# Optimization experiments

Hardware: AMD Instinct MI355X
Metric: run time of the kernel (lower is better)

Reference implementation:

```python
import jax, jax.numpy as jnp
import numpy as np

N, E, D, H = 50000, 800000, 64, 4


def setup_inputs() -> dict:
    key = jax.random.key(0)
    ks = jax.random.split(key, 12)
    w = lambda k, shape: jax.random.normal(k, shape, jnp.float32) * 0.05
    return {
        "nfeats": jax.random.normal(ks[0], (N, D), jnp.float32),
        "efeats": jax.random.normal(ks[1], (E, D), jnp.float32),
        "src": jax.random.randint(ks[2], (E,), 0, N),
        "dst": jax.random.randint(ks[3], (E,), 0, N),
        "W_ni": w(ks[4], (D, H * D)),
        "W_nj": w(ks[5], (D, H * D)),
        "W_fij": w(ks[6], (D, H * D)),
        "bias_e": jnp.zeros((H * D,), jnp.float32),
        "attn": w(ks[7], (H, D)),
        "W_src": w(ks[8], (D, H * D)),
        "W_mlp_node": w(ks[9], (H * D, D)),
        "b_mlp_node": jnp.zeros((D,), jnp.float32),
        "W_mlp_edge": w(ks[10], (H * D, D)),
        "b_mlp_edge": jnp.zeros((D,), jnp.float32),
    }


def reference(nfeats, efeats, src, dst, W_ni, W_nj, W_fij, bias_e, attn,
              W_src, W_mlp_node, b_mlp_node, W_mlp_edge, b_mlp_edge):
    n, d = nfeats.shape
    h = attn.shape[0]
    # DGL EGATConv: edge logits from src node, dst node and edge features
    f_ni = (nfeats @ W_ni)[src]            # [E, H*D] gather src
    f_nj = (nfeats @ W_nj)[dst]            # [E, H*D] gather dst
    f_fij = efeats @ W_fij                 # [E, H*D]
    f_out = jax.nn.leaky_relu(f_ni + f_nj + f_fij + bias_e, 0.01)
    f_out = f_out.reshape(-1, h, d)        # [E, H, D] new edge feats
    e = jnp.einsum('ehd,hd->eh', f_out, attn)  # [E, H] attention logits
    # edge softmax over incoming edges of each dst node
    e_max = jax.ops.segment_max(e, dst, num_segments=n)
    e_exp = jnp.exp(e - e_max[dst])
    denom = jax.ops.segment_sum(e_exp, dst, num_segments=n)
    a = e_exp / denom[dst]                 # [E, H]
    # weighted message passing: scatter-sum to dst
    h_src = (nfeats @ W_src).reshape(n, h, d)[src]  # [E, H, D]
    h_out = jax.ops.segment_sum(h_src * a[:, :, None], dst, num_segments=n)  # [N, H, D]
    # EGATLayer head-mixing MLPs + ELU
    node = jax.nn.elu(h_out.reshape(n, h * d) @ W_mlp_node + b_mlp_node)
    edge = jax.nn.elu(f_out.reshape(-1, h * d) @ W_mlp_edge + b_mlp_edge)
    return node, edge
```

## Files before the change

kernel.cpp:

```cpp
#include <hip/hip_runtime.h>
#include <hip/hip_bf16.h>

#define N_NODES 50000
#define N_EDGES 800000
#define DD 64
#define HH 4
#define HD 256
#define EB 32
#define CAP 64

typedef __attribute__((ext_vector_type(8))) short bf16x8;
typedef __attribute__((ext_vector_type(4))) float f32x4;

__device__ __forceinline__ short f2bf(float x) {
  unsigned u = __builtin_bit_cast(unsigned, x);
  unsigned r = (u + 0x7fffu + ((u >> 16) & 1u)) >> 16;
  return (short)r;
}
__device__ __forceinline__ float bf2f(unsigned short u) {
  return __builtin_bit_cast(float, (unsigned)u << 16);
}

__global__ __launch_bounds__(256) void k_proj(const float* __restrict__ nfeats,
    const float* __restrict__ W_src, unsigned short* __restrict__ hsrc) {
  __shared__ __align__(16) float Wl[DD * HD];
  const float4* W4 = (const float4*)W_src;
  float4* Wl4 = (float4*)Wl;
#pragma unroll
  for (int i = 0; i < 16; ++i) Wl4[threadIdx.x + i * 256] = W4[threadIdx.x + i * 256];
  __syncthreads();
  const int wave = threadIdx.x >> 6, lane = threadIdx.x & 63;
  for (int n = blockIdx.x * 4 + wave; n < N_NODES; n += gridDim.x * 4) {
    const float4* x4 = (const float4*)(nfeats + n * DD);
    float4 acc = make_float4(0.f, 0.f, 0.f, 0.f);
#pragma unroll
    for (int k4 = 0; k4 < 16; ++k4) {
      float4 xv = x4[k4];
      const float* wr = &Wl[(k4 * 4) * HD + 4 * lane];
      float4 w0 = *(const float4*)(wr);
      float4 w1 = *(const float4*)(wr + HD);
      float4 w2 = *(const float4*)(wr + 2 * HD);
      float4 w3 = *(const float4*)(wr + 3 * HD);
      acc.x += xv.x * w0.x + xv.y * w1.x + xv.z * w2.x + xv.w * w3.x;
      acc.y += xv.x * w0.y + xv.y * w1.y + xv.z * w2.y + xv.w * w3.y;
      acc.z += xv.x * w0.z + xv.y * w1.z + xv.z * w2.z + xv.w * w3.z;
      acc.w += xv.x * w0.w + xv.y * w1.w + xv.z * w2.w + xv.w * w3.w;
    }
    short4 s;
    s.x = f2bf(acc.x); s.y = f2bf(acc.y); s.z = f2bf(acc.z); s.w = f2bf(acc.w);
    *(short4*)&hsrc[n * HD + 4 * lane] = s;
  }
}

__global__ __launch_bounds__(256, 2) void k_edge(
    const float* __restrict__ efeats, const int* __restrict__ src, const int* __restrict__ dst,
    const float* __restrict__ nfeats,
    const float* __restrict__ W_fij, const float* __restrict__ W_ni, const float* __restrict__ W_nj,
    const float* __restrict__ bias_e, const float* __restrict__ attn,
    const float* __restrict__ W_mlp_edge, const float* __restrict__ b_mlp_edge,
    float* __restrict__ eexp, float* __restrict__ edge_out) {
  __shared__ __align__(16) short a_lds[12 * 64 * 8];
  __shared__ __align__(16) short fout_lds[EB * HD];
  __shared__ __align__(16) float part[4][EB][68];

  const int t = threadIdx.x;
  const int lane = t & 63;
  const int w = t >> 6;
  const int l15 = lane & 15, l4 = lane >> 4;

  bf16x8 wcat[6][4];
#pragma unroll
  for (int ks = 0; ks < 6; ++ks) {
    const float* Wp = ks < 2 ? (W_fij + (ks * 32) * HD)
                             : (ks < 4 ? (W_ni + ((ks - 2) * 32) * HD)
                                       : (W_nj + ((ks - 4) * 32) * HD));
#pragma unroll
    for (int n = 0; n < 4; ++n) {
      bf16x8 a;
#pragma unroll
      for (int i = 0; i < 8; ++i)
        a[i] = f2bf(Wp[(l4 * 8 + i) * HD + (w * 64 + n * 16 + l15)]);
      wcat[ks][n] = a;
    }
  }
  bf16x8 wm[2][4];
#pragma unroll
  for (int ks = 0; ks < 2; ++ks)
#pragma unroll
    for (int n = 0; n < 4; ++n) {
      bf16x8 b;
#pragma unroll
      for (int i = 0; i < 8; ++i)
        b[i] = f2bf(W_mlp_edge[(w * 64 + ks * 32 + l4 * 8 + i) * 64 + (n * 16 + l15)]);
      wm[ks][n] = b;
    }
  float bias_r[4], attn_r[4];
#pragma unroll
  for (int n = 0; n < 4; ++n) {
    const int col = w * 64 + n * 16 + l15;
    bias_r[n] = bias_e[col];
    attn_r[n] = attn[col];
  }
  const int fr = t >> 3, fc = (t & 7) * 8;
  float bme_r[8];
#pragma unroll
  for (int i = 0; i < 8; ++i) bme_r[i] = b_mlp_edge[fc + i];

  for (int tile = blockIdx.x; tile < N_EDGES / EB; tile += gridDim.x) {
    const int base = tile * EB;
    {
      const int msub = fr >> 4, rr = fr & 15, kq = fc >> 5, kk = (fc >> 3) & 3;
      const int pos = rr | (kk << 4);
      const int srow = src[base + fr], drow = dst[base + fr];
      float4 x0, x1; bf16x8 p;

      x0 = *(const float4*)&efeats[(base + fr) * DD + fc];
      x1 = *(const float4*)&efeats[(base + fr) * DD + fc + 4];
      p[0] = f2bf(x0.x); p[1] = f2bf(x0.y); p[2] = f2bf(x0.z); p[3] = f2bf(x0.w);
      p[4] = f2bf(x1.x); p[5] = f2bf(x1.y); p[6] = f2bf(x1.z); p[7] = f2bf(x1.w);
      ((bf16x8*)a_lds)[(msub * 6 + kq) * 64 + pos] = p;

      x0 = *(const float4*)&nfeats[srow * DD + fc];
      x1 = *(const float4*)&nfeats[srow * DD + fc + 4];
      p[0] = f2bf(x0.x); p[1] = f2bf(x0.y); p[2] = f2bf(x0.z); p[3] = f2bf(x0.w);
      p[4] = f2bf(x1.x); p[5] = f2bf(x1.y); p[6] = f2bf(x1.z); p[7] = f2bf(x1.w);
      ((bf16x8*)a_lds)[(msub * 6 + 2 + kq) * 64 + pos] = p;

      x0 = *(const float4*)&nfeats[drow * DD + fc];
      x1 = *(const float4*)&nfeats[drow * DD + fc + 4];
      p[0] = f2bf(x0.x); p[1] = f2bf(x0.y); p[2] = f2bf(x0.z); p[3] = f2bf(x0.w);
      p[4] = f2bf(x1.x); p[5] = f2bf(x1.y); p[6] = f2bf(x1.z); p[7] = f2bf(x1.w);
      ((bf16x8*)a_lds)[(msub * 6 + 4 + kq) * 64 + pos] = p;
    }
    __syncthreads();

    f32x4 acc[2][4] = {};
#pragma unroll
    for (int m = 0; m < 2; ++m) {
      bf16x8 af[6];
#pragma unroll
      for (int ks = 0; ks < 6; ++ks)
        af[ks] = ((const bf16x8*)a_lds)[(m * 6 + ks) * 64 + lane];
#pragma unroll
      for (int n = 0; n < 4; ++n)
#pragma unroll
        for (int ks = 0; ks < 6; ++ks)
          acc[m][n] = __builtin_amdgcn_mfma_f32_16x16x32_bf16(af[ks], wcat[ks][n], acc[m][n], 0, 0, 0);
    }

#pragma unroll
    for (int m = 0; m < 2; ++m) {
#pragma unroll
      for (int reg = 0; reg < 4; ++reg) {
        const int re = m * 16 + l4 * 4 + reg;
        float p = 0.f;
#pragma unroll
        for (int n = 0; n < 4; ++n) {
          const int col = w * 64 + n * 16 + l15;
          float v = acc[m][n][reg] + bias_r[n];
          v = v >= 0.f ? v : 0.01f * v;
          p += v * attn_r[n];
          int byte = re * 512 + col * 2;
          byte ^= (re & 7) << 4;
          *(short*)((char*)fout_lds + byte) = f2bf(v);
        }
        p += __shfl_xor(p, 1, 64); p += __shfl_xor(p, 2, 64);
        p += __shfl_xor(p, 4, 64); p += __shfl_xor(p, 8, 64);
        if (l15 == 0) {
          eexp[(base + re) * 4 + w] = expf(p);
        }
      }
    }

    f32x4 acc2[2][4] = {};
#pragma unroll
    for (int m = 0; m < 2; ++m) {
      const int rr2 = m * 16 + l15;
      int byA = rr2 * 512 + (w * 64 + l4 * 8) * 2;       byA ^= (rr2 & 7) << 4;
      int byB = rr2 * 512 + (w * 64 + 32 + l4 * 8) * 2;  byB ^= (rr2 & 7) << 4;
      bf16x8 pfa = *(const bf16x8*)((char*)fout_lds + byA);
      bf16x8 pfb = *(const bf16x8*)((char*)fout_lds + byB);
#pragma unroll
      for (int n = 0; n < 4; ++n) {
        acc2[m][n] = __builtin_amdgcn_mfma_f32_16x16x32_bf16(pfa, wm[0][n], acc2[m][n], 0, 0, 0);
        acc2[m][n] = __builtin_amdgcn_mfma_f32_16x16x32_bf16(pfb, wm[1][n], acc2[m][n], 0, 0, 0);
      }
    }
#pragma unroll
    for (int m = 0; m < 2; ++m)
#pragma unroll
      for (int n = 0; n < 4; ++n)
#pragma unroll
        for (int reg = 0; reg < 4; ++reg)
          part[w][m * 16 + l4 * 4 + reg][n * 16 + l15] = acc2[m][n][reg];
    __syncthreads();

    {
      float o[8];
#pragma unroll
      for (int i = 0; i < 8; ++i)
        o[i] = part[0][fr][fc + i] + part[1][fr][fc + i] +
               part[2][fr][fc + i] + part[3][fr][fc + i] + bme_r[i];
#pragma unroll
      for (int i = 0; i < 8; ++i) o[i] = o[i] > 0.f ? o[i] : (expf(o[i]) - 1.f);
      float4 s0 = make_float4(o[0], o[1], o[2], o[3]);
      float4 s1 = make_float4(o[4], o[5], o[6], o[7]);
      *(float4*)&edge_out[(base + fr) * DD + fc] = s0;
      *(float4*)&edge_out[(base + fr) * DD + fc + 4] = s1;
    }
  }
}

__global__ __launch_bounds__(256) void k_fill(const int* __restrict__ dst,
    int* __restrict__ cnt, int* __restrict__ bucket) {
  const int e = blockIdx.x * 256 + threadIdx.x;
  if (e < N_EDGES) {
    const int d = dst[e];
    const int slot = atomicAdd(&cnt[d], 1);
    if (slot < CAP) bucket[d * CAP + slot] = e;
  }
}

__global__ __launch_bounds__(256) void k_aggc(const int* __restrict__ src,
    const int* __restrict__ cnt, const int* __restrict__ bucket,
    const float* __restrict__ eexp, const unsigned short* __restrict__ hsrc_all,
    float* __restrict__ h_out) {
  const int lane = threadIdx.x & 63;
  const int n = (blockIdx.x * 256 + threadIdx.x) >> 6;
  if (n >= N_NODES) return;
  int deg = cnt[n];
  if (deg > CAP) deg = CAP;
  float ex0 = 0.f, ex1 = 0.f, ex2 = 0.f, ex3 = 0.f;
  int s = 0;
  if (lane < deg) {
    const int e = bucket[n * CAP + lane];
    s = src[e];
    const float4 ex = *(const float4*)&eexp[e * 4];
    ex0 = ex.x; ex1 = ex.y; ex2 = ex.z; ex3 = ex.w;
  }
  float d0 = ex0, d1 = ex1, d2 = ex2, d3 = ex3;
#pragma unroll
  for (int off = 32; off; off >>= 1) {
    d0 += __shfl_xor(d0, off, 64); d1 += __shfl_xor(d1, off, 64);
    d2 += __shfl_xor(d2, off, 64); d3 += __shfl_xor(d3, off, 64);
  }
  float a0 = 0.f, a1 = 0.f, a2 = 0.f, a3 = 0.f;
  for (int i = 0; i < deg; ++i) {
    const int si = __shfl(s, i, 64);
    const float w0 = __shfl(ex0, i, 64), w1 = __shfl(ex1, i, 64);
    const float w2 = __shfl(ex2, i, 64), w3 = __shfl(ex3, i, 64);
    const unsigned short* hp = hsrc_all + (size_t)si * HD;
    a0 += w0 * bf2f(hp[lane]);
    a1 += w1 * bf2f(hp[64 + lane]);
    a2 += w2 * bf2f(hp[128 + lane]);
    a3 += w3 * bf2f(hp[192 + lane]);
  }
  float* op = h_out + (size_t)n * HD;
  op[lane]       = d0 > 0.f ? a0 / d0 : 0.f;
  op[64 + lane]  = d1 > 0.f ? a1 / d1 : 0.f;
  op[128 + lane] = d2 > 0.f ? a2 / d2 : 0.f;
  op[192 + lane] = d3 > 0.f ? a3 / d3 : 0.f;
}

__global__ __launch_bounds__(256) void k_node(const float* __restrict__ h_out,
    const float* __restrict__ W, const float* __restrict__ b, float* __restrict__ node) {
  __shared__ __align__(16) float Wl[HD * 64];
  const float4* W4 = (const float4*)W;
  float4* Wl4 = (float4*)Wl;
#pragma unroll
  for (int i = 0; i < 16; ++i) Wl4[threadIdx.x + i * 256] = W4[threadIdx.x + i * 256];
  __syncthreads();
  const int wave = threadIdx.x >> 6, lane = threadIdx.x & 63;
  const float br = b[lane];
  for (int n = blockIdx.x * 4 + wave; n < N_NODES; n += gridDim.x * 4) {
    const float4* h4 = (const float4*)(h_out + n * HD);
    float acc = 0.f;
#pragma unroll 8
    for (int k4 = 0; k4 < 64; ++k4) {
      float4 hv = h4[k4];
      acc += hv.x * Wl[(k4 * 4) * 64 + lane] + hv.y * Wl[(k4 * 4 + 1) * 64 + lane] +
             hv.z * Wl[(k4 * 4 + 2) * 64 + lane] + hv.w * Wl[(k4 * 4 + 3) * 64 + lane];
    }
    float v = acc + br;
    node[n * DD + lane] = v > 0.f ? v : (expf(v) - 1.f);
  }
}

extern "C" void kernel_launch(void* const* d_in, const int* in_sizes, int n_in,
                              void* d_out, int out_size, void* d_ws, size_t ws_size,
                              hipStream_t stream) {
  const float* nfeats     = (const float*)d_in[0];
  const float* efeats     = (const float*)d_in[1];
  const int*   src        = (const int*)d_in[2];
  const int*   dst        = (const int*)d_in[3];
  const float* W_ni       = (const float*)d_in[4];
  const float* W_nj       = (const float*)d_in[5];
  const float* W_fij      = (const float*)d_in[6];
  const float* bias_e     = (const float*)d_in[7];
  const float* attn       = (const float*)d_in[8];
  const float* W_src      = (const float*)d_in[9];
  const float* W_mlp_node = (const float*)d_in[10];
  const float* b_mlp_node = (const float*)d_in[11];
  const float* W_mlp_edge = (const float*)d_in[12];
  const float* b_mlp_edge = (const float*)d_in[13];

  float* node_out = (float*)d_out;
  float* edge_out = node_out + (size_t)N_NODES * DD;

  char* wsb = (char*)d_ws;
  unsigned short* hsrc_bf = (unsigned short*)wsb;
  float* eexp  = (float*)(wsb + 25600000);
  float* h_out = (float*)(wsb + 38400000);
  int*   cnt    = (int*)(wsb + 89600000);
  int*   bucket = (int*)(wsb + 89800000);

  k_proj<<<512, 256, 0, stream>>>(nfeats, W_src, hsrc_bf);
  k_edge<<<1024, 256, 0, stream>>>(efeats, src, dst, nfeats,
                                   W_fij, W_ni, W_nj, bias_e, attn,
                                   W_mlp_edge, b_mlp_edge, eexp, edge_out);
  hipMemsetAsync(cnt, 0, (size_t)N_NODES * sizeof(int), stream);
  k_fill<<<(N_EDGES + 255) / 256, 256, 0, stream>>>(dst, cnt, bucket);
  k_aggc<<<(N_NODES * 64 + 255) / 256, 256, 0, stream>>>(src, cnt, bucket, eexp, hsrc_bf, h_out);
  k_node<<<512, 256, 0, stream>>>(h_out, W_mlp_node, b_mlp_node, node_out);
}
```

Before: 619.8 us.

## Split edge MLP by output columns per wave, drop cross-wave partial reduction

The edge-MLP GEMM is repartitioned so each wave owns 16 output columns and runs the full K=256 reduction over the shared bf16 f_out tile. This removes the per-wave partial-sum buffer in LDS and the reduction pass over it, freeing LDS, and the launch bound is raised to 3 blocks per CU for more occupancy. The A-operand LDS layout gets an XOR swizzle to reduce bank conflicts, and bf16 conversion now uses the intrinsic. It adds a barrier before the second GEMM, and the output stores become scalar and less coalesced.

```diff
diff --git a/kernel.cpp b/kernel.cpp
--- a/kernel.cpp
+++ b/kernel.cpp
@@ -13,9 +13,7 @@
 typedef __attribute__((ext_vector_type(4))) float f32x4;
 
 __device__ __forceinline__ short f2bf(float x) {
-  unsigned u = __builtin_bit_cast(unsigned, x);
-  unsigned r = (u + 0x7fffu + ((u >> 16) & 1u)) >> 16;
-  return (short)r;
+  return __builtin_bit_cast(short, __float2bfloat16(x));
 }
 __device__ __forceinline__ float bf2f(unsigned short u) {
   return __builtin_bit_cast(float, (unsigned)u << 16);
@@ -52,7 +50,7 @@
   }
 }
 
-__global__ __launch_bounds__(256, 2) void k_edge(
+__global__ __launch_bounds__(256, 3) void k_edge(
     const float* __restrict__ efeats, const int* __restrict__ src, const int* __restrict__ dst,
     const float* __restrict__ nfeats,
     const float* __restrict__ W_fij, const float* __restrict__ W_ni, const float* __restrict__ W_nj,
@@ -61,7 +59,6 @@
     float* __restrict__ eexp, float* __restrict__ edge_out) {
   __shared__ __align__(16) short a_lds[12 * 64 * 8];
   __shared__ __align__(16) short fout_lds[EB * HD];
-  __shared__ __align__(16) float part[4][EB][68];
 
   const int t = threadIdx.x;
   const int lane = t & 63;
@@ -83,17 +80,15 @@
       wcat[ks][n] = a;
     }
   }
-  bf16x8 wm[2][4];
-#pragma unroll
-  for (int ks = 0; ks < 2; ++ks)
-#pragma unroll
-    for (int n = 0; n < 4; ++n) {
-      bf16x8 b;
-#pragma unroll
-      for (int i = 0; i < 8; ++i)
-        b[i] = f2bf(W_mlp_edge[(w * 64 + ks * 32 + l4 * 8 + i) * 64 + (n * 16 + l15)]);
-      wm[ks][n] = b;
-    }
+  bf16x8 wm[8];
+#pragma unroll
+  for (int ks = 0; ks < 8; ++ks) {
+    bf16x8 b;
+#pragma unroll
+    for (int i = 0; i < 8; ++i)
+      b[i] = f2bf(W_mlp_edge[(ks * 32 + l4 * 8 + i) * 64 + (w * 16 + l15)]);
+    wm[ks] = b;
+  }
   float bias_r[4], attn_r[4];
 #pragma unroll
   for (int n = 0; n < 4; ++n) {
@@ -101,16 +96,17 @@
     bias_r[n] = bias_e[col];
     attn_r[n] = attn[col];
   }
-  const int fr = t >> 3, fc = (t & 7) * 8;
-  float bme_r[8];
-#pragma unroll
-  for (int i = 0; i < 8; ++i) bme_r[i] = b_mlp_edge[fc + i];
+  const float bme_r = b_mlp_edge[w * 16 + l15];
+
+  const int fr = t >> 3;
+  const int c = t & 7;
+  const int fc = c * 8;
+  const int msub = fr >> 4, rr = fr & 15, kq = c >> 2, kk = c & 3;
+  const int posx = ((rr ^ c) & 15) | (kk << 4);
 
   for (int tile = blockIdx.x; tile < N_EDGES / EB; tile += gridDim.x) {
     const int base = tile * EB;
     {
-      const int msub = fr >> 4, rr = fr & 15, kq = fc >> 5, kk = (fc >> 3) & 3;
-      const int pos = rr | (kk << 4);
       const int srow = src[base + fr], drow = dst[base + fr];
       float4 x0, x1; bf16x8 p;
 
@@ -118,19 +114,19 @@
       x1 = *(const float4*)&efeats[(base + fr) * DD + fc + 4];
       p[0] = f2bf(x0.x); p[1] = f2bf(x0.y); p[2] = f2bf(x0.z); p[3] = f2bf(x0.w);
       p[4] = f2bf(x1.x); p[5] = f2bf(x1.y); p[6] = f2bf(x1.z); p[7] = f2bf(x1.w);
-      ((bf16x8*)a_lds)[(msub * 6 + kq) * 64 + pos] = p;
+      ((bf16x8*)a_lds)[(msub * 6 + kq) * 64 + posx] = p;
 
       x0 = *(const float4*)&nfeats[srow * DD + fc];
       x1 = *(const float4*)&nfeats[srow * DD + fc + 4];
       p[0] = f2bf(x0.x); p[1] = f2bf(x0.y); p[2] = f2bf(x0.z); p[3] = f2bf(x0.w);
       p[4] = f2bf(x1.x); p[5] = f2bf(x1.y); p[6] = f2bf(x1.z); p[7] = f2bf(x1.w);
-      ((bf16x8*)a_lds)[(msub * 6 + 2 + kq) * 64 + pos] = p;
+      ((bf16x8*)a_lds)[(msub * 6 + 2 + kq) * 64 + posx] = p;
 
       x0 = *(const float4*)&nfeats[drow * DD + fc];
       x1 = *(const float4*)&nfeats[drow * DD + fc + 4];
       p[0] = f2bf(x0.x); p[1] = f2bf(x0.y); p[2] = f2bf(x0.z); p[3] = f2bf(x0.w);
       p[4] = f2bf(x1.x); p[5] = f2bf(x1.y); p[6] = f2bf(x1.z); p[7] = f2bf(x1.w);
-      ((bf16x8*)a_lds)[(msub * 6 + 4 + kq) * 64 + pos] = p;
+      ((bf16x8*)a_lds)[(msub * 6 + 4 + kq) * 64 + posx] = p;
     }
     __syncthreads();
 
@@ -139,8 +135,10 @@
     for (int m = 0; m < 2; ++m) {
       bf16x8 af[6];
 #pragma unroll
-      for (int ks = 0; ks < 6; ++ks)
-        af[ks] = ((const bf16x8*)a_lds)[(m * 6 + ks) * 64 + lane];
+      for (int ks = 0; ks < 6; ++ks) {
+        const int px = (((lane & 15) ^ (((ks & 1) << 2) | (lane >> 4))) & 15) | ((lane >> 4) << 4);
+        af[ks] = ((const bf16x8*)a_lds)[(m * 6 + ks) * 64 + px];
+      }
 #pragma unroll
       for (int n = 0; n < 4; ++n)
 #pragma unroll
@@ -171,42 +169,24 @@
         }
       }
     }
-
-    f32x4 acc2[2][4] = {};
+    __syncthreads();
+
 #pragma unroll
     for (int m = 0; m < 2; ++m) {
-      const int rr2 = m * 16 + l15;
-      int byA = rr2 * 512 + (w * 64 + l4 * 8) * 2;       byA ^= (rr2 & 7) << 4;
-      int byB = rr2 * 512 + (w * 64 + 32 + l4 * 8) * 2;  byB ^= (rr2 & 7) << 4;
-      bf16x8 pfa = *(const bf16x8*)((char*)fout_lds + byA);
-      bf16x8 pfb = *(const bf16x8*)((char*)fout_lds + byB);
-#pragma unroll
-      for (int n = 0; n < 4; ++n) {
-        acc2[m][n] = __builtin_amdgcn_mfma_f32_16x16x32_bf16(pfa, wm[0][n], acc2[m][n], 0, 0, 0);
-        acc2[m][n] = __builtin_amdgcn_mfma_f32_16x16x32_bf16(pfb, wm[1][n], acc2[m][n], 0, 0, 0);
+      f32x4 acc2 = {};
+#pragma unroll
+      for (int ks = 0; ks < 8; ++ks) {
+        int byte = (m * 16 + l15) * 512 + ks * 64 + l4 * 16;
+        byte ^= (l15 & 7) << 4;
+        bf16x8 pf = *(const bf16x8*)((char*)fout_lds + byte);
+        acc2 = __builtin_amdgcn_mfma_f32_16x16x32_bf16(pf, wm[ks], acc2, 0, 0, 0);
       }
-    }
-#pragma unroll
-    for (int m = 0; m < 2; ++m)
-#pragma unroll
-      for (int n = 0; n < 4; ++n)
-#pragma unroll
-        for (int reg = 0; reg < 4; ++reg)
-          part[w][m * 16 + l4 * 4 + reg][n * 16 + l15] = acc2[m][n][reg];
-    __syncthreads();
-
-    {
-      float o[8];
-#pragma unroll
-      for (int i = 0; i < 8; ++i)
-        o[i] = part[0][fr][fc + i] + part[1][fr][fc + i] +
-               part[2][fr][fc + i] + part[3][fr][fc + i] + bme_r[i];
-#pragma unroll
-      for (int i = 0; i < 8; ++i) o[i] = o[i] > 0.f ? o[i] : (expf(o[i]) - 1.f);
-      float4 s0 = make_float4(o[0], o[1], o[2], o[3]);
-      float4 s1 = make_float4(o[4], o[5], o[6], o[7]);
-      *(float4*)&edge_out[(base + fr) * DD + fc] = s0;
-      *(float4*)&edge_out[(base + fr) * DD + fc + 4] = s1;
+#pragma unroll
+      for (int reg = 0; reg < 4; ++reg) {
+        float v = acc2[reg] + bme_r;
+        v = v > 0.f ? v : (expf(v) - 1.f);
+        edge_out[(size_t)(base + m * 16 + l4 * 4 + reg) * DD + w * 16 + l15] = v;
+      }
     }
   }
 }
```

Result: slower. 1.252 ms (+102.1%).
